# Performance work log

Hardware: AMD Instinct MI355X
Metric: run time of the kernel (lower is better)

## Reference

```python
import jax, jax.numpy as jnp
import numpy as np

ALPHA = 0.1        # self.alpha in the torch module
NUM_CLASSES = 10   # predict_acc hardcodes range(10)


def _sqdist(x, centers):
    # Faithful to sum((x - c)**2, -1) but computed via the gemm identity to
    # avoid materializing the (N, K, D) broadcast the torch code creates.
    x2 = jnp.sum(x * x, axis=1, keepdims=True)          # [N, 1]
    c2 = jnp.sum(centers * centers, axis=1)             # [K]
    d = x2 + c2[None, :] - 2.0 * (x @ centers.T)        # [N, K]
    return jnp.maximum(d, 0.0)                          # clamp fp round-off


def _predict_acc(distance, y):
    n = distance.shape[0]
    y_p = jnp.argmin(distance, axis=1)                  # index[1][:, 0]
    # counts[i, c] = #points assigned to cluster i (only i < 10 matter) with label c
    onehot_cluster = (y_p[:, None] == jnp.arange(NUM_CLASSES)[None, :]).astype(jnp.float32)  # [N, 10]
    onehot_label = (y[:, None] == jnp.arange(NUM_CLASSES)[None, :]).astype(jnp.float32)      # [N, 10]
    counts = onehot_cluster.T @ onehot_label            # [10, 10]
    used = jnp.zeros((NUM_CLASSES,), dtype=bool)
    correct = jnp.float32(0.0)
    for i in range(NUM_CLASSES):
        bin_i = counts[i]
        has_points = jnp.sum(bin_i) > 0                 # empty bincount -> 'continue'
        label = jnp.argmax(bin_i)                       # first max index, like where(bin==max)[0][0]
        # quchong: recursively zero already-used labels == argmax with used masked out
        masked = jnp.where(used, 0.0, bin_i)
        label = jnp.where(used[label], jnp.argmax(masked), label)
        correct = correct + jnp.where(has_points, bin_i[label], 0.0)
        used = jnp.where(has_points, used.at[label].set(True), used)
    return correct / jnp.float32(n)


def setup_inputs() -> dict:
    key = jax.random.key(0)
    kx, ky, kc = jax.random.split(key, 3)
    N, K, D = 262144, 256, 64
    x = jax.random.normal(kx, (N, D), dtype=jnp.float32)
    y = jax.random.randint(ky, (N,), 0, 10, dtype=jnp.int64)
    centers = jax.random.normal(kc, (K, D), dtype=jnp.float32)
    return {"x": x, "y": y, "centers": centers}


def reference(x, y, centers):
    distance = _sqdist(x, centers)                      # caldis, op='l2'
    # calwei: exp(-alpha*log(d+1)) then row-normalize
    we = jnp.exp(-ALPHA * jnp.log1p(distance))
    weight = we / jnp.sum(we, axis=1, keepdims=True)
    loss = jnp.sum(weight * distance)                   # calloss
    acc = _predict_acc(distance, y)
    return (loss, acc)
```

## Files before the change

kernel.cpp:

```cpp
#include <hip/hip_runtime.h>

#define ALPHA 0.1f
#define NUM_CLASSES 10

typedef __attribute__((ext_vector_type(8))) short bf16x8;
typedef __attribute__((ext_vector_type(4))) float f32x4;


__device__ __forceinline__ unsigned pack2(float a, float b) {
    return (__float_as_uint(b) & 0xFFFF0000u) | (__float_as_uint(a) >> 16);
}
__device__ __forceinline__ float truncbf(float a) {
    return __uint_as_float(__float_as_uint(a) & 0xFFFF0000u);
}


__global__ __launch_bounds__(512, 4) void dist_kernel(
    const float* __restrict__ x,
    const int*   __restrict__ y,
    const float* __restrict__ centers,
    float* __restrict__ loss_acc,
    unsigned int* __restrict__ counts,
    int NT)
{
    __shared__ __align__(16) char bstage[4 * 4 * 64 * 16];
    __shared__ float x2s[64];
    __shared__ float c2s[256];
    __shared__ float    comb_swe[8][64];
    __shared__ float    comb_swd[8][64];
    __shared__ unsigned comb_best[8][64];

    const int tid  = threadIdx.x;
    const int w    = tid >> 6;
    const int lane = tid & 63;
    const int q    = lane >> 4;
    const int r    = lane & 15;

    if (tid < 256) {
        const float4* crow = (const float4*)(centers + tid * 64);
        float s = 0.f;
#pragma unroll
        for (int j = 0; j < 16; ++j) {
            float4 v = crow[j];
            s = fmaf(v.x, v.x, s); s = fmaf(v.y, v.y, s);
            s = fmaf(v.z, v.z, s); s = fmaf(v.w, v.w, s);
        }
        c2s[tid] = s;
    }

    bf16x8 af[2][4];
#pragma unroll
    for (int ct = 0; ct < 2; ++ct) {
        const int row = w * 32 + ct * 16 + r;
        const float4* C = (const float4*)(centers + (size_t)row * 64);
        float4 v0 = C[q * 2], v1 = C[q * 2 + 1];
        float4 v2 = C[8 + q * 2], v3 = C[9 + q * 2];
        float4 m0 = make_float4(-2.f * v0.x, -2.f * v0.y, -2.f * v0.z, -2.f * v0.w);
        float4 m1 = make_float4(-2.f * v1.x, -2.f * v1.y, -2.f * v1.z, -2.f * v1.w);
        float4 m2 = make_float4(-2.f * v2.x, -2.f * v2.y, -2.f * v2.z, -2.f * v2.w);
        float4 m3 = make_float4(-2.f * v3.x, -2.f * v3.y, -2.f * v3.z, -2.f * v3.w);
        union { bf16x8 v; unsigned u[4]; } h0, h1, l0, l1;
        h0.u[0] = pack2(m0.x, m0.y); h0.u[1] = pack2(m0.z, m0.w);
        h0.u[2] = pack2(m1.x, m1.y); h0.u[3] = pack2(m1.z, m1.w);
        h1.u[0] = pack2(m2.x, m2.y); h1.u[1] = pack2(m2.z, m2.w);
        h1.u[2] = pack2(m3.x, m3.y); h1.u[3] = pack2(m3.z, m3.w);
        l0.u[0] = pack2(m0.x - truncbf(m0.x), m0.y - truncbf(m0.y));
        l0.u[1] = pack2(m0.z - truncbf(m0.z), m0.w - truncbf(m0.w));
        l0.u[2] = pack2(m1.x - truncbf(m1.x), m1.y - truncbf(m1.y));
        l0.u[3] = pack2(m1.z - truncbf(m1.z), m1.w - truncbf(m1.w));
        l1.u[0] = pack2(m2.x - truncbf(m2.x), m2.y - truncbf(m2.y));
        l1.u[1] = pack2(m2.z - truncbf(m2.z), m2.w - truncbf(m2.w));
        l1.u[2] = pack2(m3.x - truncbf(m3.x), m3.y - truncbf(m3.y));
        l1.u[3] = pack2(m3.z - truncbf(m3.z), m3.w - truncbf(m3.w));
        af[ct][0] = h0.v; af[ct][1] = h1.v; af[ct][2] = l0.v; af[ct][3] = l1.v;
    }

    float4 pv0, pv1, pv2, pv3;
    if (w < 4) {
        const int row = blockIdx.x * 64 + w * 16 + r;
        const float4* X = (const float4*)(x + (size_t)row * 64);
        pv0 = X[q * 2]; pv1 = X[q * 2 + 1];
        pv2 = X[8 + q * 2]; pv3 = X[9 + q * 2];
    }

    __syncthreads();

    float c2r1[2][4];
#pragma unroll
    for (int ct = 0; ct < 2; ++ct) {
        float4 v = *(const float4*)(c2s + w * 32 + ct * 16 + q * 4);
        c2r1[ct][0] = v.x + 1.f; c2r1[ct][1] = v.y + 1.f;
        c2r1[ct][2] = v.z + 1.f; c2r1[ct][3] = v.w + 1.f;
    }

    float loss_local = 0.f;

    for (int t = blockIdx.x; t < NT; t += gridDim.x) {
        int ylab = 0;
        if (tid < 64) ylab = y[t * 64 + tid];

        if (w < 4) {
            float4 v0 = pv0, v1 = pv1, v2 = pv2, v3 = pv3;

            const int tn = t + gridDim.x;
            if (tn < NT) {
                const int row = tn * 64 + w * 16 + r;
                const float4* X = (const float4*)(x + (size_t)row * 64);
                pv0 = X[q * 2]; pv1 = X[q * 2 + 1];
                pv2 = X[8 + q * 2]; pv3 = X[9 + q * 2];
            }

            float p = v0.x * v0.x;
            p = fmaf(v0.y, v0.y, p); p = fmaf(v0.z, v0.z, p); p = fmaf(v0.w, v0.w, p);
            p = fmaf(v1.x, v1.x, p); p = fmaf(v1.y, v1.y, p); p = fmaf(v1.z, v1.z, p); p = fmaf(v1.w, v1.w, p);
            p = fmaf(v2.x, v2.x, p); p = fmaf(v2.y, v2.y, p); p = fmaf(v2.z, v2.z, p); p = fmaf(v2.w, v2.w, p);
            p = fmaf(v3.x, v3.x, p); p = fmaf(v3.y, v3.y, p); p = fmaf(v3.z, v3.z, p); p = fmaf(v3.w, v3.w, p);
            p += __shfl_xor(p, 16);
            p += __shfl_xor(p, 32);
            if (q == 0) x2s[w * 16 + r] = p;

            union { bf16x8 v; uint4 u4; unsigned u[4]; } h0, h1, l0, l1;
            h0.u[0] = pack2(v0.x, v0.y); h0.u[1] = pack2(v0.z, v0.w);
            h0.u[2] = pack2(v1.x, v1.y); h0.u[3] = pack2(v1.z, v1.w);
            h1.u[0] = pack2(v2.x, v2.y); h1.u[1] = pack2(v2.z, v2.w);
            h1.u[2] = pack2(v3.x, v3.y); h1.u[3] = pack2(v3.z, v3.w);
            l0.u[0] = pack2(v0.x - truncbf(v0.x), v0.y - truncbf(v0.y));
            l0.u[1] = pack2(v0.z - truncbf(v0.z), v0.w - truncbf(v0.w));
            l0.u[2] = pack2(v1.x - truncbf(v1.x), v1.y - truncbf(v1.y));
            l0.u[3] = pack2(v1.z - truncbf(v1.z), v1.w - truncbf(v1.w));
            l1.u[0] = pack2(v2.x - truncbf(v2.x), v2.y - truncbf(v2.y));
            l1.u[1] = pack2(v2.z - truncbf(v2.z), v2.w - truncbf(v2.w));
            l1.u[2] = pack2(v3.x - truncbf(v3.x), v3.y - truncbf(v3.y));
            l1.u[3] = pack2(v3.z - truncbf(v3.z), v3.w - truncbf(v3.w));
            *(uint4*)(bstage + (((w * 4 + 0) * 64 + lane) << 4)) = h0.u4;
            *(uint4*)(bstage + (((w * 4 + 1) * 64 + lane) << 4)) = h1.u4;
            *(uint4*)(bstage + (((w * 4 + 2) * 64 + lane) << 4)) = l0.u4;
            *(uint4*)(bstage + (((w * 4 + 3) * 64 + lane) << 4)) = l1.u4;
        }
        __syncthreads();

#pragma unroll
        for (int pt = 0; pt < 4; ++pt) {
            union { uint4 u4; bf16x8 v; } b0, b1, b2, b3;
            b0.u4 = *(const uint4*)(bstage + (((pt * 4 + 0) * 64 + lane) << 4));
            b1.u4 = *(const uint4*)(bstage + (((pt * 4 + 1) * 64 + lane) << 4));
            b2.u4 = *(const uint4*)(bstage + (((pt * 4 + 2) * 64 + lane) << 4));
            b3.u4 = *(const uint4*)(bstage + (((pt * 4 + 3) * 64 + lane) << 4));
            const float x2p = x2s[pt * 16 + r];

            f32x4 acc[2];
#pragma unroll
            for (int ct = 0; ct < 2; ++ct) {
                f32x4 a;
                a[0] = x2p + c2r1[ct][0]; a[1] = x2p + c2r1[ct][1];
                a[2] = x2p + c2r1[ct][2]; a[3] = x2p + c2r1[ct][3];
                a = __builtin_amdgcn_mfma_f32_16x16x32_bf16(af[ct][0], b0.v, a, 0, 0, 0);
                a = __builtin_amdgcn_mfma_f32_16x16x32_bf16(af[ct][1], b1.v, a, 0, 0, 0);
                a = __builtin_amdgcn_mfma_f32_16x16x32_bf16(af[ct][2], b0.v, a, 0, 0, 0);
                a = __builtin_amdgcn_mfma_f32_16x16x32_bf16(af[ct][3], b1.v, a, 0, 0, 0);
                a = __builtin_amdgcn_mfma_f32_16x16x32_bf16(af[ct][0], b2.v, a, 0, 0, 0);
                a = __builtin_amdgcn_mfma_f32_16x16x32_bf16(af[ct][1], b3.v, a, 0, 0, 0);
                acc[ct] = a;
            }

            float swe = 0.f, swdu = 0.f;
            unsigned best = 0xFFFFFFFFu;
#pragma unroll
            for (int ct = 0; ct < 2; ++ct) {
#pragma unroll
                for (int reg = 0; reg < 4; ++reg) {
                    const float u = acc[ct][reg];
                    const unsigned kid = (unsigned)(w * 32 + ct * 16 + q * 4 + reg);
                    best = min(best, (__float_as_uint(u) & 0xFFFFFF00u) | kid);
                    float wg = exp2f(-ALPHA * __log2f(u));
                    swe += wg;
                    swdu = fmaf(wg, u, swdu);
                }
            }
            swe += __shfl_xor(swe, 16); swe += __shfl_xor(swe, 32);
            swdu += __shfl_xor(swdu, 16); swdu += __shfl_xor(swdu, 32);
            best = min(best, (unsigned)__shfl_xor((int)best, 16));
            best = min(best, (unsigned)__shfl_xor((int)best, 32));
            if (q == 0) {
                comb_swe[w][pt * 16 + r] = swe;
                comb_swd[w][pt * 16 + r] = swdu;
                comb_best[w][pt * 16 + r] = best;
            }
        }
        __syncthreads();

        if (tid < 64) {
            float SWE = comb_swe[0][tid], SWD = comb_swd[0][tid];
            unsigned BEST = comb_best[0][tid];
#pragma unroll
            for (int g = 1; g < 8; ++g) {
                SWE += comb_swe[g][tid];
                SWD += comb_swd[g][tid];
                BEST = min(BEST, comb_best[g][tid]);
            }
            loss_local += SWD / SWE - 1.f;
            const unsigned bk = BEST & 0xFFu;
            if (bk < NUM_CLASSES) {
                atomicAdd(&counts[bk * NUM_CLASSES + ylab], 1u);
            }
        }
    }

    if (w == 0) {
        float v = loss_local;
#pragma unroll
        for (int o = 32; o > 0; o >>= 1) v += __shfl_down(v, o);
        if (lane == 0) atomicAdd(loss_acc, v);
    }
}


__global__ void finalize_kernel(
    const float* __restrict__ loss_acc,
    const unsigned int* __restrict__ counts,
    float* __restrict__ out,
    int N)
{
    if (threadIdx.x == 0 && blockIdx.x == 0) {
        float c[NUM_CLASSES][NUM_CLASSES];
        for (int i = 0; i < NUM_CLASSES; ++i)
            for (int j = 0; j < NUM_CLASSES; ++j)
                c[i][j] = (float)counts[i * NUM_CLASSES + j];

        bool used[NUM_CLASSES];
        for (int i = 0; i < NUM_CLASSES; ++i) used[i] = false;

        float correct = 0.f;
        for (int i = 0; i < NUM_CLASSES; ++i) {
            float rowsum = 0.f;
            for (int j = 0; j < NUM_CLASSES; ++j) rowsum += c[i][j];
            bool has_points = rowsum > 0.f;

            int label = 0;
            float mx = c[i][0];
            for (int j = 1; j < NUM_CLASSES; ++j)
                if (c[i][j] > mx) { mx = c[i][j]; label = j; }

            if (used[label]) {
                float mm = used[0] ? 0.f : c[i][0];
                int l2 = 0;
                for (int j = 1; j < NUM_CLASSES; ++j) {
                    float v = used[j] ? 0.f : c[i][j];
                    if (v > mm) { mm = v; l2 = j; }
                }
                label = l2;
            }

            if (has_points) {
                correct += c[i][label];
                used[label] = true;
            }
        }
        out[0] = loss_acc[0];
        out[1] = correct / (float)N;
    }
}


extern "C" void kernel_launch(void* const* d_in, const int* in_sizes, int n_in,
                              void* d_out, int out_size, void* d_ws, size_t ws_size,
                              hipStream_t stream)
{
    const float* x       = (const float*)d_in[0];
    const int*   y       = (const int*)d_in[1];
    const float* centers = (const float*)d_in[2];
    float* out = (float*)d_out;

    const int N  = in_sizes[0] / 64;
    const int NT = N / 64;

    float* loss          = (float*)d_ws;
    unsigned int* counts = (unsigned int*)((char*)d_ws + 4);

    hipMemsetAsync(d_ws, 0, 512, stream);

    int grid = 1024;
    if (grid > NT) grid = NT;
    dist_kernel<<<grid, 512, 0, stream>>>(x, y, centers, loss, counts, NT);

    finalize_kernel<<<1, 64, 0, stream>>>(loss, counts, out, N);
}
```

Before: 151.9 us.

## Give each wave its own point tile across all centers, drop per-tile block syncs

Each wave now owns 16 points and loops over all 256 centers, reading the pre-split bf16 hi/lo center fragments from shared memory. Previously waves split the centers and combined partial results through shared memory with two barriers per tile. Per-block cluster/label counts go into shared-memory atomics and are flushed to global once at the end. Tiles are 128 points and the grid is halved. This removes per-tile __syncthreads and cross-wave reductions, at the cost of more LDS reads for the A fragments each iteration and a large 64KB shared buffer that may limit occupancy.

```diff
diff --git a/kernel.cpp b/kernel.cpp
--- a/kernel.cpp
+++ b/kernel.cpp
@@ -13,7 +13,6 @@
 __device__ __forceinline__ float truncbf(float a) {
     return __uint_as_float(__float_as_uint(a) & 0xFFFF0000u);
 }
-
 
 __global__ __launch_bounds__(512, 4) void dist_kernel(
     const float* __restrict__ x,
@@ -23,18 +22,17 @@
     unsigned int* __restrict__ counts,
     int NT)
 {
-    __shared__ __align__(16) char bstage[4 * 4 * 64 * 16];
-    __shared__ float x2s[64];
-    __shared__ float c2s[256];
-    __shared__ float    comb_swe[8][64];
-    __shared__ float    comb_swd[8][64];
-    __shared__ unsigned comb_best[8][64];
-
-    const int tid  = threadIdx.x;
-    const int w    = tid >> 6;
-    const int lane = tid & 63;
-    const int q    = lane >> 4;
-    const int r    = lane & 15;
+    __shared__ __align__(16) char afr[16 * 4 * 64 * 16];
+    __shared__ float c2s1[256];
+    __shared__ unsigned int counts_l[100];
+
+    const int tid = threadIdx.x;
+    const int w   = tid >> 6;
+    const int l   = tid & 63;
+    const int pr  = l & 15;
+    const int kg  = l >> 4;
+
+    if (tid < 100) counts_l[tid] = 0u;
 
     if (tid < 256) {
         const float4* crow = (const float4*)(centers + tid * 64);
@@ -45,172 +43,142 @@
             s = fmaf(v.x, v.x, s); s = fmaf(v.y, v.y, s);
             s = fmaf(v.z, v.z, s); s = fmaf(v.w, v.w, s);
         }
-        c2s[tid] = s;
-    }
-
-    bf16x8 af[2][4];
-#pragma unroll
-    for (int ct = 0; ct < 2; ++ct) {
-        const int row = w * 32 + ct * 16 + r;
-        const float4* C = (const float4*)(centers + (size_t)row * 64);
-        float4 v0 = C[q * 2], v1 = C[q * 2 + 1];
-        float4 v2 = C[8 + q * 2], v3 = C[9 + q * 2];
-        float4 m0 = make_float4(-2.f * v0.x, -2.f * v0.y, -2.f * v0.z, -2.f * v0.w);
-        float4 m1 = make_float4(-2.f * v1.x, -2.f * v1.y, -2.f * v1.z, -2.f * v1.w);
-        float4 m2 = make_float4(-2.f * v2.x, -2.f * v2.y, -2.f * v2.z, -2.f * v2.w);
-        float4 m3 = make_float4(-2.f * v3.x, -2.f * v3.y, -2.f * v3.z, -2.f * v3.w);
-        union { bf16x8 v; unsigned u[4]; } h0, h1, l0, l1;
-        h0.u[0] = pack2(m0.x, m0.y); h0.u[1] = pack2(m0.z, m0.w);
-        h0.u[2] = pack2(m1.x, m1.y); h0.u[3] = pack2(m1.z, m1.w);
-        h1.u[0] = pack2(m2.x, m2.y); h1.u[1] = pack2(m2.z, m2.w);
-        h1.u[2] = pack2(m3.x, m3.y); h1.u[3] = pack2(m3.z, m3.w);
-        l0.u[0] = pack2(m0.x - truncbf(m0.x), m0.y - truncbf(m0.y));
-        l0.u[1] = pack2(m0.z - truncbf(m0.z), m0.w - truncbf(m0.w));
-        l0.u[2] = pack2(m1.x - truncbf(m1.x), m1.y - truncbf(m1.y));
-        l0.u[3] = pack2(m1.z - truncbf(m1.z), m1.w - truncbf(m1.w));
-        l1.u[0] = pack2(m2.x - truncbf(m2.x), m2.y - truncbf(m2.y));
-        l1.u[1] = pack2(m2.z - truncbf(m2.z), m2.w - truncbf(m2.w));
-        l1.u[2] = pack2(m3.x - truncbf(m3.x), m3.y - truncbf(m3.y));
-        l1.u[3] = pack2(m3.z - truncbf(m3.z), m3.w - truncbf(m3.w));
-        af[ct][0] = h0.v; af[ct][1] = h1.v; af[ct][2] = l0.v; af[ct][3] = l1.v;
-    }
-
+        c2s1[tid] = s + 1.f;
+    }
+
+#pragma unroll
+    for (int it = 0; it < 4; ++it) {
+        const int idx = (it << 9) | tid;
+        const int ct  = idx >> 3;
+        const int c8  = idx & 7;
+        const int g   = ct >> 4;
+        const int kgg = c8 & 3;
+        const int fhi = c8 >> 2;
+        const int lc  = (ct & 15) | (kgg << 4);
+        const float4* C = (const float4*)(centers + (size_t)ct * 64);
+        const float4 v0 = C[c8 * 2];
+        const float4 v1 = C[c8 * 2 + 1];
+        const float m0x = -2.f * v0.x, m0y = -2.f * v0.y;
+        const float m0z = -2.f * v0.z, m0w = -2.f * v0.w;
+        const float m1x = -2.f * v1.x, m1y = -2.f * v1.y;
+        const float m1z = -2.f * v1.z, m1w = -2.f * v1.w;
+        uint4 hi, lo;
+        hi.x = pack2(m0x, m0y); hi.y = pack2(m0z, m0w);
+        hi.z = pack2(m1x, m1y); hi.w = pack2(m1z, m1w);
+        lo.x = pack2(m0x - truncbf(m0x), m0y - truncbf(m0y));
+        lo.y = pack2(m0z - truncbf(m0z), m0w - truncbf(m0w));
+        lo.z = pack2(m1x - truncbf(m1x), m1y - truncbf(m1y));
+        lo.w = pack2(m1z - truncbf(m1z), m1w - truncbf(m1w));
+        *(uint4*)(afr + ((((g << 2) + fhi)     * 64 + lc) << 4)) = hi;
+        *(uint4*)(afr + ((((g << 2) + fhi + 2) * 64 + lc) << 4)) = lo;
+    }
+
+    __syncthreads();
+
+    const int stride = gridDim.x;
+    int t = blockIdx.x;
     float4 pv0, pv1, pv2, pv3;
-    if (w < 4) {
-        const int row = blockIdx.x * 64 + w * 16 + r;
-        const float4* X = (const float4*)(x + (size_t)row * 64);
-        pv0 = X[q * 2]; pv1 = X[q * 2 + 1];
-        pv2 = X[8 + q * 2]; pv3 = X[9 + q * 2];
-    }
+    int ylab;
+    {
+        const size_t row = (size_t)(t * 128 + w * 16 + pr);
+        const float4* X = (const float4*)(x + row * 64);
+        pv0 = X[kg * 2]; pv1 = X[kg * 2 + 1];
+        pv2 = X[8 + kg * 2]; pv3 = X[9 + kg * 2];
+        ylab = y[t * 128 + w * 16 + pr];
+    }
+
+    float loss_local = 0.f;
+
+    for (; t < NT; t += stride) {
+        const float4 v0 = pv0, v1 = pv1, v2 = pv2, v3 = pv3;
+        const int yl = ylab;
+
+        const int tn = t + stride;
+        if (tn < NT) {
+            const size_t row = (size_t)(tn * 128 + w * 16 + pr);
+            const float4* X = (const float4*)(x + row * 64);
+            pv0 = X[kg * 2]; pv1 = X[kg * 2 + 1];
+            pv2 = X[8 + kg * 2]; pv3 = X[9 + kg * 2];
+            ylab = y[tn * 128 + w * 16 + pr];
+        }
+
+        float p = v0.x * v0.x;
+        p = fmaf(v0.y, v0.y, p); p = fmaf(v0.z, v0.z, p); p = fmaf(v0.w, v0.w, p);
+        p = fmaf(v1.x, v1.x, p); p = fmaf(v1.y, v1.y, p); p = fmaf(v1.z, v1.z, p); p = fmaf(v1.w, v1.w, p);
+        p = fmaf(v2.x, v2.x, p); p = fmaf(v2.y, v2.y, p); p = fmaf(v2.z, v2.z, p); p = fmaf(v2.w, v2.w, p);
+        p = fmaf(v3.x, v3.x, p); p = fmaf(v3.y, v3.y, p); p = fmaf(v3.z, v3.z, p); p = fmaf(v3.w, v3.w, p);
+        p += __shfl_xor(p, 16);
+        p += __shfl_xor(p, 32);
+
+        union { bf16x8 v; unsigned u[4]; } b0, b1, b2, b3;
+        b0.u[0] = pack2(v0.x, v0.y); b0.u[1] = pack2(v0.z, v0.w);
+        b0.u[2] = pack2(v1.x, v1.y); b0.u[3] = pack2(v1.z, v1.w);
+        b1.u[0] = pack2(v2.x, v2.y); b1.u[1] = pack2(v2.z, v2.w);
+        b1.u[2] = pack2(v3.x, v3.y); b1.u[3] = pack2(v3.z, v3.w);
+        b2.u[0] = pack2(v0.x - truncbf(v0.x), v0.y - truncbf(v0.y));
+        b2.u[1] = pack2(v0.z - truncbf(v0.z), v0.w - truncbf(v0.w));
+        b2.u[2] = pack2(v1.x - truncbf(v1.x), v1.y - truncbf(v1.y));
+        b2.u[3] = pack2(v1.z - truncbf(v1.z), v1.w - truncbf(v1.w));
+        b3.u[0] = pack2(v2.x - truncbf(v2.x), v2.y - truncbf(v2.y));
+        b3.u[1] = pack2(v2.z - truncbf(v2.z), v2.w - truncbf(v2.w));
+        b3.u[2] = pack2(v3.x - truncbf(v3.x), v3.y - truncbf(v3.y));
+        b3.u[3] = pack2(v3.z - truncbf(v3.z), v3.w - truncbf(v3.w));
+
+        float swe = 0.f, swd = 0.f;
+        unsigned best = 0xFFFFFFFFu;
+
+#pragma unroll
+        for (int g = 0; g < 16; ++g) {
+            const uint4* A = (const uint4*)(afr + (g << 12)) + l;
+            union { uint4 u4; bf16x8 v; } a0, a1, a2, a3;
+            a0.u4 = A[0];   a1.u4 = A[64];
+            a2.u4 = A[128]; a3.u4 = A[192];
+            const float4 cq = *(const float4*)(c2s1 + g * 16 + kg * 4);
+
+            f32x4 acc;
+            acc[0] = p + cq.x; acc[1] = p + cq.y;
+            acc[2] = p + cq.z; acc[3] = p + cq.w;
+            acc = __builtin_amdgcn_mfma_f32_16x16x32_bf16(a0.v, b0.v, acc, 0, 0, 0);
+            acc = __builtin_amdgcn_mfma_f32_16x16x32_bf16(a1.v, b1.v, acc, 0, 0, 0);
+            acc = __builtin_amdgcn_mfma_f32_16x16x32_bf16(a2.v, b0.v, acc, 0, 0, 0);
+            acc = __builtin_amdgcn_mfma_f32_16x16x32_bf16(a3.v, b1.v, acc, 0, 0, 0);
+            acc = __builtin_amdgcn_mfma_f32_16x16x32_bf16(a0.v, b2.v, acc, 0, 0, 0);
+            acc = __builtin_amdgcn_mfma_f32_16x16x32_bf16(a1.v, b3.v, acc, 0, 0, 0);
+
+#pragma unroll
+            for (int reg = 0; reg < 4; ++reg) {
+                const float u = acc[reg];
+                const unsigned kid = (unsigned)((g << 4) | (kg << 2) | reg);
+                best = min(best, (__float_as_uint(u) & 0xFFFFFF00u) | kid);
+                float wg = exp2f(-ALPHA * __log2f(u));
+                swe += wg;
+                swd = fmaf(wg, u, swd);
+            }
+        }
+
+        swe += __shfl_xor(swe, 16); swe += __shfl_xor(swe, 32);
+        swd += __shfl_xor(swd, 16); swd += __shfl_xor(swd, 32);
+        best = min(best, (unsigned)__shfl_xor((int)best, 16));
+        best = min(best, (unsigned)__shfl_xor((int)best, 32));
+
+        if (kg == 0) {
+            loss_local += swd / swe - 1.f;
+            const unsigned bk = best & 0xFFu;
+            if (bk < NUM_CLASSES) {
+                atomicAdd(&counts_l[bk * NUM_CLASSES + yl], 1u);
+            }
+        }
+    }
+
+    float v = loss_local;
+#pragma unroll
+    for (int o = 32; o > 0; o >>= 1) v += __shfl_down(v, o);
+    if (l == 0) atomicAdd(loss_acc, v);
 
     __syncthreads();
-
-    float c2r1[2][4];
-#pragma unroll
-    for (int ct = 0; ct < 2; ++ct) {
-        float4 v = *(const float4*)(c2s + w * 32 + ct * 16 + q * 4);
-        c2r1[ct][0] = v.x + 1.f; c2r1[ct][1] = v.y + 1.f;
-        c2r1[ct][2] = v.z + 1.f; c2r1[ct][3] = v.w + 1.f;
-    }
-
-    float loss_local = 0.f;
-
-    for (int t = blockIdx.x; t < NT; t += gridDim.x) {
-        int ylab = 0;
-        if (tid < 64) ylab = y[t * 64 + tid];
-
-        if (w < 4) {
-            float4 v0 = pv0, v1 = pv1, v2 = pv2, v3 = pv3;
-
-            const int tn = t + gridDim.x;
-            if (tn < NT) {
-                const int row = tn * 64 + w * 16 + r;
-                const float4* X = (const float4*)(x + (size_t)row * 64);
-                pv0 = X[q * 2]; pv1 = X[q * 2 + 1];
-                pv2 = X[8 + q * 2]; pv3 = X[9 + q * 2];
-            }
-
-            float p = v0.x * v0.x;
-            p = fmaf(v0.y, v0.y, p); p = fmaf(v0.z, v0.z, p); p = fmaf(v0.w, v0.w, p);
-            p = fmaf(v1.x, v1.x, p); p = fmaf(v1.y, v1.y, p); p = fmaf(v1.z, v1.z, p); p = fmaf(v1.w, v1.w, p);
-            p = fmaf(v2.x, v2.x, p); p = fmaf(v2.y, v2.y, p); p = fmaf(v2.z, v2.z, p); p = fmaf(v2.w, v2.w, p);
-            p = fmaf(v3.x, v3.x, p); p = fmaf(v3.y, v3.y, p); p = fmaf(v3.z, v3.z, p); p = fmaf(v3.w, v3.w, p);
-            p += __shfl_xor(p, 16);
-            p += __shfl_xor(p, 32);
-            if (q == 0) x2s[w * 16 + r] = p;
-
-            union { bf16x8 v; uint4 u4; unsigned u[4]; } h0, h1, l0, l1;
-            h0.u[0] = pack2(v0.x, v0.y); h0.u[1] = pack2(v0.z, v0.w);
-            h0.u[2] = pack2(v1.x, v1.y); h0.u[3] = pack2(v1.z, v1.w);
-            h1.u[0] = pack2(v2.x, v2.y); h1.u[1] = pack2(v2.z, v2.w);
-            h1.u[2] = pack2(v3.x, v3.y); h1.u[3] = pack2(v3.z, v3.w);
-            l0.u[0] = pack2(v0.x - truncbf(v0.x), v0.y - truncbf(v0.y));
-            l0.u[1] = pack2(v0.z - truncbf(v0.z), v0.w - truncbf(v0.w));
-            l0.u[2] = pack2(v1.x - truncbf(v1.x), v1.y - truncbf(v1.y));
-            l0.u[3] = pack2(v1.z - truncbf(v1.z), v1.w - truncbf(v1.w));
-            l1.u[0] = pack2(v2.x - truncbf(v2.x), v2.y - truncbf(v2.y));
-            l1.u[1] = pack2(v2.z - truncbf(v2.z), v2.w - truncbf(v2.w));
-            l1.u[2] = pack2(v3.x - truncbf(v3.x), v3.y - truncbf(v3.y));
-            l1.u[3] = pack2(v3.z - truncbf(v3.z), v3.w - truncbf(v3.w));
-            *(uint4*)(bstage + (((w * 4 + 0) * 64 + lane) << 4)) = h0.u4;
-            *(uint4*)(bstage + (((w * 4 + 1) * 64 + lane) << 4)) = h1.u4;
-            *(uint4*)(bstage + (((w * 4 + 2) * 64 + lane) << 4)) = l0.u4;
-            *(uint4*)(bstage + (((w * 4 + 3) * 64 + lane) << 4)) = l1.u4;
-        }
-        __syncthreads();
-
-#pragma unroll
-        for (int pt = 0; pt < 4; ++pt) {
-            union { uint4 u4; bf16x8 v; } b0, b1, b2, b3;
-            b0.u4 = *(const uint4*)(bstage + (((pt * 4 + 0) * 64 + lane) << 4));
-            b1.u4 = *(const uint4*)(bstage + (((pt * 4 + 1) * 64 + lane) << 4));
-            b2.u4 = *(const uint4*)(bstage + (((pt * 4 + 2) * 64 + lane) << 4));
-            b3.u4 = *(const uint4*)(bstage + (((pt * 4 + 3) * 64 + lane) << 4));
-            const float x2p = x2s[pt * 16 + r];
-
-            f32x4 acc[2];
-#pragma unroll
-            for (int ct = 0; ct < 2; ++ct) {
-                f32x4 a;
-                a[0] = x2p + c2r1[ct][0]; a[1] = x2p + c2r1[ct][1];
-                a[2] = x2p + c2r1[ct][2]; a[3] = x2p + c2r1[ct][3];
-                a = __builtin_amdgcn_mfma_f32_16x16x32_bf16(af[ct][0], b0.v, a, 0, 0, 0);
-                a = __builtin_amdgcn_mfma_f32_16x16x32_bf16(af[ct][1], b1.v, a, 0, 0, 0);
-                a = __builtin_amdgcn_mfma_f32_16x16x32_bf16(af[ct][2], b0.v, a, 0, 0, 0);
-                a = __builtin_amdgcn_mfma_f32_16x16x32_bf16(af[ct][3], b1.v, a, 0, 0, 0);
-                a = __builtin_amdgcn_mfma_f32_16x16x32_bf16(af[ct][0], b2.v, a, 0, 0, 0);
-                a = __builtin_amdgcn_mfma_f32_16x16x32_bf16(af[ct][1], b3.v, a, 0, 0, 0);
-                acc[ct] = a;
-            }
-
-            float swe = 0.f, swdu = 0.f;
-            unsigned best = 0xFFFFFFFFu;
-#pragma unroll
-            for (int ct = 0; ct < 2; ++ct) {
-#pragma unroll
-                for (int reg = 0; reg < 4; ++reg) {
-                    const float u = acc[ct][reg];
-                    const unsigned kid = (unsigned)(w * 32 + ct * 16 + q * 4 + reg);
-                    best = min(best, (__float_as_uint(u) & 0xFFFFFF00u) | kid);
-                    float wg = exp2f(-ALPHA * __log2f(u));
-                    swe += wg;
-                    swdu = fmaf(wg, u, swdu);
-                }
-            }
-            swe += __shfl_xor(swe, 16); swe += __shfl_xor(swe, 32);
-            swdu += __shfl_xor(swdu, 16); swdu += __shfl_xor(swdu, 32);
-            best = min(best, (unsigned)__shfl_xor((int)best, 16));
-            best = min(best, (unsigned)__shfl_xor((int)best, 32));
-            if (q == 0) {
-                comb_swe[w][pt * 16 + r] = swe;
-                comb_swd[w][pt * 16 + r] = swdu;
-                comb_best[w][pt * 16 + r] = best;
-            }
-        }
-        __syncthreads();
-
-        if (tid < 64) {
-            float SWE = comb_swe[0][tid], SWD = comb_swd[0][tid];
-            unsigned BEST = comb_best[0][tid];
-#pragma unroll
-            for (int g = 1; g < 8; ++g) {
-                SWE += comb_swe[g][tid];
-                SWD += comb_swd[g][tid];
-                BEST = min(BEST, comb_best[g][tid]);
-            }
-            loss_local += SWD / SWE - 1.f;
-            const unsigned bk = BEST & 0xFFu;
-            if (bk < NUM_CLASSES) {
-                atomicAdd(&counts[bk * NUM_CLASSES + ylab], 1u);
-            }
-        }
-    }
-
-    if (w == 0) {
-        float v = loss_local;
-#pragma unroll
-        for (int o = 32; o > 0; o >>= 1) v += __shfl_down(v, o);
-        if (lane == 0) atomicAdd(loss_acc, v);
+    if (tid < 100) {
+        const unsigned c = counts_l[tid];
+        if (c) atomicAdd(&counts[tid], c);
     }
 }
 
@@ -272,14 +240,14 @@
     float* out = (float*)d_out;
 
     const int N  = in_sizes[0] / 64;
-    const int NT = N / 64;
+    const int NT = N / 128;
 
     float* loss          = (float*)d_ws;
     unsigned int* counts = (unsigned int*)((char*)d_ws + 4);
 
     hipMemsetAsync(d_ws, 0, 512, stream);
 
-    int grid = 1024;
+    int grid = 512;
     if (grid > NT) grid = NT;
     dist_kernel<<<grid, 512, 0, stream>>>(x, y, centers, loss, counts, NT);
 
```

Result: slower. 355.7 us (+134.1%).

## Double points per tile, use LDS atomics for cross-wave reduction and counts

Applied to the files above, without the earlier changes.

Each block tile now covers 128 points instead of 64, so all 8 waves load and convert x rather than only half of them. The per-wave partial results are combined with LDS atomics (add and min) into 128-entry arrays instead of an 8x64 staging array followed by a serial 8-way reduction. The class-count histogram is also accumulated in a shared-memory copy and flushed to global memory once per block. This cuts idle waves during staging and reduces global atomic traffic, at the cost of LDS atomic contention, float-atomic ordering nondeterminism, and extra reset stores each iteration.

```diff
diff --git a/kernel.cpp b/kernel.cpp
--- a/kernel.cpp
+++ b/kernel.cpp
@@ -13,7 +13,6 @@
 __device__ __forceinline__ float truncbf(float a) {
     return __uint_as_float(__float_as_uint(a) & 0xFFFF0000u);
 }
-
 
 __global__ __launch_bounds__(512, 4) void dist_kernel(
     const float* __restrict__ x,
@@ -23,18 +22,24 @@
     unsigned int* __restrict__ counts,
     int NT)
 {
-    __shared__ __align__(16) char bstage[4 * 4 * 64 * 16];
-    __shared__ float x2s[64];
+    __shared__ __align__(16) char bstage[8 * 4 * 64 * 16];
+    __shared__ float x2s[128];
     __shared__ float c2s[256];
-    __shared__ float    comb_swe[8][64];
-    __shared__ float    comb_swd[8][64];
-    __shared__ unsigned comb_best[8][64];
+    __shared__ float    comb_swe[128];
+    __shared__ float    comb_swd[128];
+    __shared__ unsigned comb_best[128];
+    __shared__ unsigned counts_l[100];
 
     const int tid  = threadIdx.x;
     const int w    = tid >> 6;
     const int lane = tid & 63;
     const int q    = lane >> 4;
     const int r    = lane & 15;
+
+    if (tid < 100) counts_l[tid] = 0u;
+    if (tid < 128) {
+        comb_swe[tid] = 0.f; comb_swd[tid] = 0.f; comb_best[tid] = 0xFFFFFFFFu;
+    }
 
     if (tid < 256) {
         const float4* crow = (const float4*)(centers + tid * 64);
@@ -76,8 +81,8 @@
     }
 
     float4 pv0, pv1, pv2, pv3;
-    if (w < 4) {
-        const int row = blockIdx.x * 64 + w * 16 + r;
+    {
+        const int row = blockIdx.x * 128 + w * 16 + r;
         const float4* X = (const float4*)(x + (size_t)row * 64);
         pv0 = X[q * 2]; pv1 = X[q * 2 + 1];
         pv2 = X[8 + q * 2]; pv3 = X[9 + q * 2];
@@ -97,14 +102,14 @@
 
     for (int t = blockIdx.x; t < NT; t += gridDim.x) {
         int ylab = 0;
-        if (tid < 64) ylab = y[t * 64 + tid];
-
-        if (w < 4) {
+        if (tid < 128) ylab = y[t * 128 + tid];
+
+        {
             float4 v0 = pv0, v1 = pv1, v2 = pv2, v3 = pv3;
 
             const int tn = t + gridDim.x;
             if (tn < NT) {
-                const int row = tn * 64 + w * 16 + r;
+                const int row = tn * 128 + w * 16 + r;
                 const float4* X = (const float4*)(x + (size_t)row * 64);
                 pv0 = X[q * 2]; pv1 = X[q * 2 + 1];
                 pv2 = X[8 + q * 2]; pv3 = X[9 + q * 2];
@@ -140,7 +145,7 @@
         __syncthreads();
 
 #pragma unroll
-        for (int pt = 0; pt < 4; ++pt) {
+        for (int pt = 0; pt < 8; ++pt) {
             union { uint4 u4; bf16x8 v; } b0, b1, b2, b3;
             b0.u4 = *(const uint4*)(bstage + (((pt * 4 + 0) * 64 + lane) << 4));
             b1.u4 = *(const uint4*)(bstage + (((pt * 4 + 1) * 64 + lane) << 4));
@@ -182,35 +187,37 @@
             best = min(best, (unsigned)__shfl_xor((int)best, 16));
             best = min(best, (unsigned)__shfl_xor((int)best, 32));
             if (q == 0) {
-                comb_swe[w][pt * 16 + r] = swe;
-                comb_swd[w][pt * 16 + r] = swdu;
-                comb_best[w][pt * 16 + r] = best;
+                atomicAdd(&comb_swe[pt * 16 + r], swe);
+                atomicAdd(&comb_swd[pt * 16 + r], swdu);
+                atomicMin(&comb_best[pt * 16 + r], best);
             }
         }
         __syncthreads();
 
-        if (tid < 64) {
-            float SWE = comb_swe[0][tid], SWD = comb_swd[0][tid];
-            unsigned BEST = comb_best[0][tid];
-#pragma unroll
-            for (int g = 1; g < 8; ++g) {
-                SWE += comb_swe[g][tid];
-                SWD += comb_swd[g][tid];
-                BEST = min(BEST, comb_best[g][tid]);
-            }
+        if (tid < 128) {
+            const float SWE = comb_swe[tid];
+            const float SWD = comb_swd[tid];
+            const unsigned BEST = comb_best[tid];
             loss_local += SWD / SWE - 1.f;
             const unsigned bk = BEST & 0xFFu;
             if (bk < NUM_CLASSES) {
-                atomicAdd(&counts[bk * NUM_CLASSES + ylab], 1u);
-            }
-        }
-    }
-
-    if (w == 0) {
+                atomicAdd(&counts_l[bk * NUM_CLASSES + ylab], 1u);
+            }
+            comb_swe[tid] = 0.f; comb_swd[tid] = 0.f; comb_best[tid] = 0xFFFFFFFFu;
+        }
+    }
+
+    if (w < 2) {
         float v = loss_local;
 #pragma unroll
         for (int o = 32; o > 0; o >>= 1) v += __shfl_down(v, o);
         if (lane == 0) atomicAdd(loss_acc, v);
+    }
+
+    __syncthreads();
+    if (tid < 100) {
+        const unsigned c = counts_l[tid];
+        if (c) atomicAdd(&counts[tid], c);
     }
 }
 
@@ -272,7 +279,7 @@
     float* out = (float*)d_out;
 
     const int N  = in_sizes[0] / 64;
-    const int NT = N / 64;
+    const int NT = N / 128;
 
     float* loss          = (float*)d_ws;
     unsigned int* counts = (unsigned int*)((char*)d_ws + 4);
```

Result: slower. 160.4 us (+5.6%).
